# Performance work log

Measured on AMD Instinct MI355X. Metric: run time of the kernel, lower is better.

## Reference

```python
import jax, jax.numpy as jnp
import numpy as np

V, D, S, NL, B, L = 50257, 768, 16, 4, 2, 512
EPS = 1e-5

def _ln(x, g, b):
    m = x.mean(-1, keepdims=True)
    v = x.var(-1, keepdims=True)
    return (x - m) * jax.lax.rsqrt(v + EPS) * g + b

def setup_inputs() -> dict:
    key = jax.random.key(0)
    ks = jax.random.split(key, 10)
    def nrm(k, shape, s=0.02):
        return jax.random.normal(k, shape, jnp.float32) * s
    tokens = jax.random.randint(ks[0], (B, L), 0, V)
    return {
        "tokens": tokens,
        "emb": nrm(ks[1], (V, D)),
        "ln_g": jnp.ones((NL, D), jnp.float32),
        "ln_b": jnp.zeros((NL, D), jnp.float32),
        "in_w": nrm(ks[2], (NL, 2 * D, D)),        # torch Linear weight [out,in]
        "conv_w": nrm(ks[3], (NL, D, 3), 0.3),     # depthwise conv kernel [D,1,3] -> [D,3]
        "conv_b": jnp.zeros((NL, D), jnp.float32),
        "dt_w": nrm(ks[4], (NL, D, D)),
        "dt_b": jnp.zeros((NL, D), jnp.float32),
        "A_log": jax.random.normal(ks[5], (NL, D, S), jnp.float32),
        "D_param": jnp.ones((NL, D), jnp.float32),
        "out_w": nrm(ks[6], (NL, D, D)),
        "lnf_g": jnp.ones((D,), jnp.float32),
        "lnf_b": jnp.zeros((D,), jnp.float32),
        "head_w": nrm(ks[7], (V, D)),
    }

def _mamba_layer(x, p):
    g, b, inw, cw, cb, dtw, dtb, Al, Dd, ow = p
    xn = _ln(x, g, b)
    xr = jnp.einsum('bld,ed->ble', xn, inw)          # [B,L,2D]
    xi, res = xr[..., :D], xr[..., D:]
    # depthwise conv1d, kernel=3, padding=1 (cross-correlation, as torch)
    xp = jnp.pad(xi, ((0, 0), (1, 1), (0, 0)))
    xc = xp[:, :-2] * cw[:, 0] + xp[:, 1:-1] * cw[:, 1] + xp[:, 2:] * cw[:, 2] + cb
    xc = jax.nn.silu(xc)                              # [B,L,D]
    A = -jnp.exp(Al)                                  # [D,S]
    dt = jax.nn.sigmoid(jnp.einsum('bld,ed->ble', xc, dtw) + dtb)  # [B,L,D]
    decay = jnp.exp(A[None, None] * dt[..., None])    # [B,L,D,S]
    dec_t = jnp.moveaxis(decay, 1, 0)                 # [L,B,D,S]
    xc_t = jnp.moveaxis(xc, 1, 0)                     # [L,B,D]
    h0 = jnp.zeros((x.shape[0], D, S), x.dtype)
    def step(h, inp):
        dec, xt = inp
        h = h * dec + xt[..., None]
        return h, h.sum(-1)
    _, ys = jax.lax.scan(step, h0, (dec_t, xc_t))     # ys: [L,B,D]
    y = jnp.moveaxis(ys, 0, 1) * Dd                   # [B,L,D]
    y = y * jax.nn.silu(res)
    out = jnp.einsum('bld,ed->ble', y, ow)
    return x + out, None

def reference(tokens, emb, ln_g, ln_b, in_w, conv_w, conv_b, dt_w, dt_b,
              A_log, D_param, out_w, lnf_g, lnf_b, head_w):
    x = emb[tokens]                                   # [B,L,D]
    params = (ln_g, ln_b, in_w, conv_w, conv_b, dt_w, dt_b, A_log, D_param, out_w)
    x, _ = jax.lax.scan(_mamba_layer, x, params)      # scan over NL layers
    x = _ln(x, lnf_g, lnf_b)
    return jnp.einsum('bld,vd->blv', x, head_w)       # [B,L,V]
```

## Files before the change

### kernel.cpp

```cpp
#include <hip/hip_runtime.h>
#include <math.h>

#define V_  50257
#define D_  768
#define S_  16
#define NL_ 4
#define B_  2
#define L_  512
#define EPS_ 1e-5f

static constexpr int BLD  = B_ * L_ * D_;
static constexpr int ROWS = B_ * L_;
static constexpr int VPAD = 50304;

typedef __bf16 bf16x8 __attribute__((ext_vector_type(8)));
typedef __bf16 bf16x4 __attribute__((ext_vector_type(4)));
typedef float  f32x4  __attribute__((ext_vector_type(4)));

__global__ __launch_bounds__(256)
void emb_kernel(const int* __restrict__ tok, const float* __restrict__ emb,
                float* __restrict__ x) {
    int i = blockIdx.x * 256 + threadIdx.x;
    if (i >= BLD) return;
    int d  = i % D_;
    int bl = i / D_;
    x[i] = emb[(size_t)tok[bl] * D_ + d];
}

__global__ __launch_bounds__(256)
void ln_split_kernel(const float* __restrict__ x, const float* __restrict__ g,
                     const float* __restrict__ b, __bf16* __restrict__ hi,
                     __bf16* __restrict__ lo) {
    int row = blockIdx.x;
    const float* xr = x + (size_t)row * D_;
    int t = threadIdx.x;
    float v0 = xr[t], v1 = xr[t + 256], v2 = xr[t + 512];
    float s1 = v0 + v1 + v2;
    float s2 = v0 * v0 + v1 * v1 + v2 * v2;
    for (int off = 32; off > 0; off >>= 1) {
        s1 += __shfl_down(s1, off);
        s2 += __shfl_down(s2, off);
    }
    __shared__ float red[8];
    __shared__ float mv[2];
    int wave = t >> 6, lane = t & 63;
    if (lane == 0) { red[wave] = s1; red[4 + wave] = s2; }
    __syncthreads();
    if (t == 0) {
        float a = red[0] + red[1] + red[2] + red[3];
        float c = red[4] + red[5] + red[6] + red[7];
        float mean = a / (float)D_;
        float var  = c / (float)D_ - mean * mean;
        mv[0] = mean;
        mv[1] = 1.f / sqrtf(var + EPS_);
    }
    __syncthreads();
    float mean = mv[0], inv = mv[1];
    size_t o = (size_t)row * D_;
#pragma unroll
    for (int q = 0; q < 3; ++q) {
        int c = t + q * 256;
        float v = (q == 0 ? v0 : q == 1 ? v1 : v2);
        float n = (v - mean) * inv * g[c] + b[c];
        __bf16 h = (__bf16)n;
        hi[o + c] = h;
        lo[o + c] = (__bf16)(n - (float)h);
    }
}

__global__ __launch_bounds__(256)
void ln_kernel(const float* __restrict__ x, const float* __restrict__ g,
               const float* __restrict__ b, float* __restrict__ o) {
    int row = blockIdx.x;
    const float* xr = x + (size_t)row * D_;
    int t = threadIdx.x;
    float v0 = xr[t], v1 = xr[t + 256], v2 = xr[t + 512];
    float s1 = v0 + v1 + v2;
    float s2 = v0 * v0 + v1 * v1 + v2 * v2;
    for (int off = 32; off > 0; off >>= 1) {
        s1 += __shfl_down(s1, off);
        s2 += __shfl_down(s2, off);
    }
    __shared__ float red[8];
    __shared__ float mv[2];
    int wave = t >> 6, lane = t & 63;
    if (lane == 0) { red[wave] = s1; red[4 + wave] = s2; }
    __syncthreads();
    if (t == 0) {
        float a = red[0] + red[1] + red[2] + red[3];
        float c = red[4] + red[5] + red[6] + red[7];
        float mean = a / (float)D_;
        float var  = c / (float)D_ - mean * mean;
        mv[0] = mean;
        mv[1] = 1.f / sqrtf(var + EPS_);
    }
    __syncthreads();
    float mean = mv[0], inv = mv[1];
    float* orow = o + (size_t)row * D_;
    orow[t]       = (v0 - mean) * inv * g[t]       + b[t];
    orow[t + 256] = (v1 - mean) * inv * g[t + 256] + b[t + 256];
    orow[t + 512] = (v2 - mean) * inv * g[t + 512] + b[t + 512];
}

__global__ __launch_bounds__(256)
void conv_silu_split_kernel(const float* __restrict__ xr, const float* __restrict__ cw,
                            const float* __restrict__ cb, float* __restrict__ xc,
                            __bf16* __restrict__ hi, __bf16* __restrict__ lo) {
    int i = blockIdx.x * 256 + threadIdx.x;
    if (i >= BLD) return;
    int d  = i % D_;
    int bl = i / D_;
    int l  = bl % L_;
    const size_t stride = 2 * D_;
    float xm = (l > 0)      ? xr[(size_t)(bl - 1) * stride + d] : 0.f;
    float x0 =                xr[(size_t)bl * stride + d];
    float xp = (l < L_ - 1) ? xr[(size_t)(bl + 1) * stride + d] : 0.f;
    float v = xm * cw[d * 3 + 0] + x0 * cw[d * 3 + 1] + xp * cw[d * 3 + 2] + cb[d];
    float s = v / (1.f + __expf(-v));
    xc[i] = s;
    __bf16 h = (__bf16)s;
    hi[i] = h;
    lo[i] = (__bf16)(s - (float)h);
}

__global__ __launch_bounds__(256)
void conv_silu_kernel(const float* __restrict__ xr, const float* __restrict__ cw,
                      const float* __restrict__ cb, float* __restrict__ xc) {
    int i = blockIdx.x * 256 + threadIdx.x;
    if (i >= BLD) return;
    int d  = i % D_;
    int bl = i / D_;
    int l  = bl % L_;
    const size_t stride = 2 * D_;
    float xm = (l > 0)      ? xr[(size_t)(bl - 1) * stride + d] : 0.f;
    float x0 =                xr[(size_t)bl * stride + d];
    float xp = (l < L_ - 1) ? xr[(size_t)(bl + 1) * stride + d] : 0.f;
    float v = xm * cw[d * 3 + 0] + x0 * cw[d * 3 + 1] + xp * cw[d * 3 + 2] + cb[d];
    xc[i] = v / (1.f + __expf(-v));
}

__global__ __launch_bounds__(256)
void scan2_kernel(const float* __restrict__ dt, const float* __restrict__ xc,
                  const float* __restrict__ xr, const float* __restrict__ A_log,
                  const float* __restrict__ Dp, __bf16* __restrict__ yh,
                  __bf16* __restrict__ yl) {
    const int tid = threadIdx.x;
    const int s  = tid & 15;
    const int dd = (tid >> 4) & 1;
    const int c  = tid >> 5;
    const int dg = blockIdx.x % (D_ / 2);
    const int b  = blockIdx.x / (D_ / 2);
    const int d  = dg * 2 + dd;
    const float a = -__expf(A_log[d * S_ + s]);
    const int l0 = c * (L_ / 8);
    const float* dtp = dt + (size_t)b * L_ * D_ + d;
    const float* xcp = xc + (size_t)b * L_ * D_ + d;

    float P = 1.f, H = 0.f;
#pragma unroll 4
    for (int i = 0; i < L_ / 8; ++i) {
        float dtv = dtp[(size_t)(l0 + i) * D_];
        float xcv = xcp[(size_t)(l0 + i) * D_];
        float dec = __expf(a * dtv);
        P *= dec;
        H = H * dec + xcv;
    }
    __shared__ float Ps[8][2][16], Hs[8][2][16], HIn[8][2][16];
    Ps[c][dd][s] = P;
    Hs[c][dd][s] = H;
    __syncthreads();
    if (tid < 32) {
        int ss = tid & 15, d2 = tid >> 4;
        float carry = 0.f;
#pragma unroll
        for (int cc = 0; cc < 8; ++cc) {
            HIn[cc][d2][ss] = carry;
            carry = Hs[cc][d2][ss] + Ps[cc][d2][ss] * carry;
        }
    }
    __syncthreads();
    float h = HIn[c][dd][s];
    const float Dd = Dp[d];
    const float* rsp = xr + (size_t)b * L_ * 2 * D_ + D_ + d;
    size_t ybase = (size_t)b * L_ * D_ + d;
#pragma unroll 4
    for (int i = 0; i < L_ / 8; ++i) {
        int l = l0 + i;
        float dtv = dtp[(size_t)l * D_];
        float xcv = xcp[(size_t)l * D_];
        h = h * __expf(a * dtv) + xcv;
        float ys = h;
        ys += __shfl_xor(ys, 1, 16);
        ys += __shfl_xor(ys, 2, 16);
        ys += __shfl_xor(ys, 4, 16);
        ys += __shfl_xor(ys, 8, 16);
        if (s == 0) {
            float rv = rsp[(size_t)l * 2 * D_];
            float sil = rv / (1.f + __expf(-rv));
            float val = ys * Dd * sil;
            __bf16 hh = (__bf16)val;
            yh[ybase + (size_t)l * D_] = hh;
            yl[ybase + (size_t)l * D_] = (__bf16)(val - (float)hh);
        }
    }
}

__global__ __launch_bounds__(256)
void scan_kernel(const float* __restrict__ dt, const float* __restrict__ xc,
                 const float* __restrict__ xr, const float* __restrict__ A_log,
                 const float* __restrict__ Dp, float* __restrict__ y) {
    int t = blockIdx.x * 256 + threadIdx.x;
    int s = t & (S_ - 1);
    int d = (t >> 4) % D_;
    int b = t / (D_ * S_);
    float a  = -__expf(A_log[d * S_ + s]);
    float Dd = Dp[d];
    const float* dtp = dt + (size_t)b * L_ * D_ + d;
    const float* xcp = xc + (size_t)b * L_ * D_ + d;
    const float* rsp = xr + (size_t)b * L_ * 2 * D_ + D_ + d;
    float* yp = y + (size_t)b * L_ * D_ + d;
    float h = 0.f;
    for (int l = 0; l < L_; ++l) {
        float dtv = dtp[(size_t)l * D_];
        float xcv = xcp[(size_t)l * D_];
        h = h * __expf(a * dtv) + xcv;
        float ys = h;
        ys += __shfl_xor(ys, 1, 16);
        ys += __shfl_xor(ys, 2, 16);
        ys += __shfl_xor(ys, 4, 16);
        ys += __shfl_xor(ys, 8, 16);
        if (s == 0) {
            float rv = rsp[(size_t)l * 2 * D_];
            float sil = rv / (1.f + __expf(-rv));
            yp[(size_t)l * D_] = ys * Dd * sil;
        }
    }
}

__global__ __launch_bounds__(256)
void split4_kernel(const float* __restrict__ x, __bf16* __restrict__ hi,
                   __bf16* __restrict__ lo, int n4, int npad4) {
    int i = blockIdx.x * 256 + threadIdx.x;
    if (i >= npad4) return;
    float4 v = {0.f, 0.f, 0.f, 0.f};
    if (i < n4) v = ((const float4*)x)[i];
    bf16x4 h, l;
    h[0] = (__bf16)v.x; h[1] = (__bf16)v.y; h[2] = (__bf16)v.z; h[3] = (__bf16)v.w;
    l[0] = (__bf16)(v.x - (float)h[0]);
    l[1] = (__bf16)(v.y - (float)h[1]);
    l[2] = (__bf16)(v.z - (float)h[2]);
    l[3] = (__bf16)(v.w - (float)h[3]);
    *(bf16x4*)&hi[(size_t)i * 4] = h;
    *(bf16x4*)&lo[(size_t)i * 4] = l;
}

template <int BMt, int BNt, int EPI>
__global__ __launch_bounds__(256)
void gemm3(const __bf16* __restrict__ Ahi, const __bf16* __restrict__ Alo,
           const __bf16* __restrict__ Whi, const __bf16* __restrict__ Wlo,
           const float* __restrict__ bias, const float* __restrict__ resid,
           float* __restrict__ C, int N, int K, int gx) {
    constexpr int BK  = 32;
    constexpr int FR  = BMt / 32;
    constexpr int FC  = BNt / 32;
    constexpr int ASZ = BMt * BK;
    constexpr int WSZ = BNt * BK;
    __shared__ __bf16 Ah[2 * ASZ];
    __shared__ __bf16 Al[2 * ASZ];
    __shared__ __bf16 Wh[2 * WSZ];
    __shared__ __bf16 Wl[2 * WSZ];
    const int tid  = threadIdx.x;
    const int lane = tid & 63;
    const int wv   = tid >> 6;
    const int wr   = wv >> 1, wc = wv & 1;

    const int bid = blockIdx.x;
    const int nwg = gridDim.x;
    const int q = nwg >> 3, r = nwg & 7;
    const int xcd = bid & 7, lid = bid >> 3;
    const int swz = (xcd < r ? xcd * (q + 1) : r * (q + 1) + (xcd - r) * q) + lid;
    const int bm = (swz % gx) * BMt;
    const int bn = (swz / gx) * BNt;

    const int srow = tid >> 2;
    const int scol = (tid & 3) * 8;

    f32x4 acc[FR][FC] = {};

    const int arow = wr * (BMt / 2) + (lane & 15);
    const int brow = wc * (BNt / 2) + (lane & 15);
    const int kof  = (lane >> 4) * 8;

    auto STAGE = [&](int t) {
        const int k0  = t * BK;
        const int buf = t & 1;
#pragma unroll
        for (int i = 0; i < BMt / 64; ++i) {
            size_t go = (size_t)(bm + i * 64 + srow) * K + k0 + scol;
            __builtin_amdgcn_global_load_lds(
                (const __attribute__((address_space(1))) void*)(Ahi + go),
                (__attribute__((address_space(3))) void*)(Ah + buf * ASZ + i * 2048 + tid * 8),
                16, 0, 0);
            __builtin_amdgcn_global_load_lds(
                (const __attribute__((address_space(1))) void*)(Alo + go),
                (__attribute__((address_space(3))) void*)(Al + buf * ASZ + i * 2048 + tid * 8),
                16, 0, 0);
        }
#pragma unroll
        for (int i = 0; i < BNt / 64; ++i) {
            size_t go = (size_t)(bn + i * 64 + srow) * K + k0 + scol;
            __builtin_amdgcn_global_load_lds(
                (const __attribute__((address_space(1))) void*)(Whi + go),
                (__attribute__((address_space(3))) void*)(Wh + buf * WSZ + i * 2048 + tid * 8),
                16, 0, 0);
            __builtin_amdgcn_global_load_lds(
                (const __attribute__((address_space(1))) void*)(Wlo + go),
                (__attribute__((address_space(3))) void*)(Wl + buf * WSZ + i * 2048 + tid * 8),
                16, 0, 0);
        }
    };

    STAGE(0);
    const int nt = K / BK;
    for (int t = 0; t < nt; ++t) {
        __syncthreads();
        if (t + 1 < nt) STAGE(t + 1);
        const int buf = t & 1;
        const __bf16* Ahb = Ah + buf * ASZ;
        const __bf16* Alb = Al + buf * ASZ;
        const __bf16* Whb = Wh + buf * WSZ;
        const __bf16* Wlb = Wl + buf * WSZ;

        bf16x8 afh[FR], afl[FR], wfh[FC], wfl[FC];
#pragma unroll
        for (int f = 0; f < FR; ++f) {
            afh[f] = *(const bf16x8*)&Ahb[(arow + f * 16) * BK + kof];
            afl[f] = *(const bf16x8*)&Alb[(arow + f * 16) * BK + kof];
        }
#pragma unroll
        for (int f = 0; f < FC; ++f) {
            wfh[f] = *(const bf16x8*)&Whb[(brow + f * 16) * BK + kof];
            wfl[f] = *(const bf16x8*)&Wlb[(brow + f * 16) * BK + kof];
        }
#pragma unroll
        for (int i = 0; i < FR; ++i)
#pragma unroll
            for (int j = 0; j < FC; ++j) {
                acc[i][j] = __builtin_amdgcn_mfma_f32_16x16x32_bf16(
                    afh[i], wfh[j], acc[i][j], 0, 0, 0);
                acc[i][j] = __builtin_amdgcn_mfma_f32_16x16x32_bf16(
                    afl[i], wfh[j], acc[i][j], 0, 0, 0);
                acc[i][j] = __builtin_amdgcn_mfma_f32_16x16x32_bf16(
                    afh[i], wfl[j], acc[i][j], 0, 0, 0);
            }
    }

    const int rbase = bm + wr * (BMt / 2) + (lane >> 4) * 4;
    const int cbase = bn + wc * (BNt / 2) + (lane & 15);
#pragma unroll
    for (int i = 0; i < FR; ++i) {
#pragma unroll
        for (int j = 0; j < FC; ++j) {
#pragma unroll
            for (int r2 = 0; r2 < 4; ++r2) {
                int row = rbase + i * 16 + r2;
                int col = cbase + j * 16;
                if (col < N) {
                    float v = acc[i][j][r2];
                    if (EPI == 1) v = 1.f / (1.f + __expf(-(v + bias[col])));
                    if (EPI == 2) v = v + resid[(size_t)row * N + col];
                    C[(size_t)row * N + col] = v;
                }
            }
        }
    }
}

#define BM 128
#define BN 128
#define BKF 16

template <int EPI>
__global__ __launch_bounds__(256)
void gemm_wt(const float* __restrict__ A, const float* __restrict__ W,
             const float* __restrict__ bias, const float* __restrict__ resid,
             float* __restrict__ C, int M, int N, int K) {
    __shared__ float As[BKF][BM + 4];
    __shared__ float Wsh[BKF][BN + 4];
    const int tid = threadIdx.x;
    const int bm = blockIdx.y * BM;
    const int bn = blockIdx.x * BN;
    const int tx = tid & 15, ty = tid >> 4;
    const int lrow = tid >> 1;
    const int lk   = (tid & 1) * 8;
    float acc[8][8];
#pragma unroll
    for (int i = 0; i < 8; ++i)
#pragma unroll
        for (int j = 0; j < 8; ++j) acc[i][j] = 0.f;
    for (int k0 = 0; k0 < K; k0 += BKF) {
        const float* ap = A + (size_t)(bm + lrow) * K + k0 + lk;
        float4 av0 = *(const float4*)ap;
        float4 av1 = *(const float4*)(ap + 4);
        float4 wv0 = {0, 0, 0, 0}, wv1 = {0, 0, 0, 0};
        int wrow = bn + lrow;
        if (wrow < N) {
            const float* wp = W + (size_t)wrow * K + k0 + lk;
            wv0 = *(const float4*)wp;
            wv1 = *(const float4*)(wp + 4);
        }
        __syncthreads();
        As[lk + 0][lrow] = av0.x; As[lk + 1][lrow] = av0.y;
        As[lk + 2][lrow] = av0.z; As[lk + 3][lrow] = av0.w;
        As[lk + 4][lrow] = av1.x; As[lk + 5][lrow] = av1.y;
        As[lk + 6][lrow] = av1.z; As[lk + 7][lrow] = av1.w;
        Wsh[lk + 0][lrow] = wv0.x; Wsh[lk + 1][lrow] = wv0.y;
        Wsh[lk + 2][lrow] = wv0.z; Wsh[lk + 3][lrow] = wv0.w;
        Wsh[lk + 4][lrow] = wv1.x; Wsh[lk + 5][lrow] = wv1.y;
        Wsh[lk + 6][lrow] = wv1.z; Wsh[lk + 7][lrow] = wv1.w;
        __syncthreads();
#pragma unroll
        for (int k = 0; k < BKF; ++k) {
            float4 a0 = *(const float4*)&As[k][ty * 8];
            float4 a1 = *(const float4*)&As[k][ty * 8 + 4];
            float4 w0 = *(const float4*)&Wsh[k][tx * 8];
            float4 w1 = *(const float4*)&Wsh[k][tx * 8 + 4];
            float av[8] = {a0.x, a0.y, a0.z, a0.w, a1.x, a1.y, a1.z, a1.w};
            float wv[8] = {w0.x, w0.y, w0.z, w0.w, w1.x, w1.y, w1.z, w1.w};
#pragma unroll
            for (int i = 0; i < 8; ++i)
#pragma unroll
                for (int j = 0; j < 8; ++j)
                    acc[i][j] = fmaf(av[i], wv[j], acc[i][j]);
        }
    }
#pragma unroll
    for (int i = 0; i < 8; ++i) {
        int row = bm + ty * 8 + i;
#pragma unroll
        for (int j = 0; j < 8; ++j) {
            int col = bn + tx * 8 + j;
            if (col < N) {
                float v = acc[i][j];
                if (EPI == 1) v = 1.f / (1.f + expf(-(v + bias[col])));
                if (EPI == 2) v = v + resid[(size_t)row * N + col];
                C[(size_t)row * N + col] = v;
            }
        }
    }
}

extern "C" void kernel_launch(void* const* d_in, const int* in_sizes, int n_in,
                              void* d_out, int out_size, void* d_ws, size_t ws_size,
                              hipStream_t stream) {
    (void)in_sizes; (void)n_in; (void)out_size;
    const int*   tokens  = (const int*)  d_in[0];
    const float* emb     = (const float*)d_in[1];
    const float* ln_g    = (const float*)d_in[2];
    const float* ln_b    = (const float*)d_in[3];
    const float* in_w    = (const float*)d_in[4];
    const float* conv_w  = (const float*)d_in[5];
    const float* conv_b  = (const float*)d_in[6];
    const float* dt_w    = (const float*)d_in[7];
    const float* dt_b    = (const float*)d_in[8];
    const float* A_log   = (const float*)d_in[9];
    const float* D_param = (const float*)d_in[10];
    const float* out_w   = (const float*)d_in[11];
    const float* lnf_g   = (const float*)d_in[12];
    const float* lnf_b   = (const float*)d_in[13];
    const float* head_w  = (const float*)d_in[14];
    float* out = (float*)d_out;

    char* base = (char*)d_ws;
    char* p = base;
    auto alloc = [&](size_t bytes) -> char* {
        char* r = p;
        p += (bytes + 255) & ~(size_t)255;
        return r;
    };
    float* x  = (float*)alloc((size_t)BLD * 4);
    float* xn = (float*)alloc((size_t)BLD * 4);
    float* xr = (float*)alloc((size_t)2 * BLD * 4);
    float* xc = (float*)alloc((size_t)BLD * 4);
    float* dt = (float*)alloc((size_t)BLD * 4);
    float* y  = xn;
    size_t fb_need = (size_t)(p - base);

    __bf16* a_hi = (__bf16*)alloc((size_t)BLD * 2);
    __bf16* a_lo = (__bf16*)alloc((size_t)BLD * 2);
    const size_t INW = (size_t)NL_ * 2 * D_ * D_;
    const size_t SQW = (size_t)NL_ * D_ * D_;
    const size_t HW  = (size_t)VPAD * D_;
    __bf16* inw_hi  = (__bf16*)alloc(INW * 2);
    __bf16* inw_lo  = (__bf16*)alloc(INW * 2);
    __bf16* dtw_hi  = (__bf16*)alloc(SQW * 2);
    __bf16* dtw_lo  = (__bf16*)alloc(SQW * 2);
    __bf16* outw_hi = (__bf16*)alloc(SQW * 2);
    __bf16* outw_lo = (__bf16*)alloc(SQW * 2);
    __bf16* hw_hi   = (__bf16*)alloc(HW * 2);
    __bf16* hw_lo   = (__bf16*)alloc(HW * 2);
    size_t fast_need = (size_t)(p - base);

    const bool fast = ws_size >= fast_need && fb_need <= ws_size;

    emb_kernel<<<(BLD + 255) / 256, 256, 0, stream>>>(tokens, emb, x);

    if (fast) {
        int n4;
        n4 = (int)(INW / 4);
        split4_kernel<<<(n4 + 255) / 256, 256, 0, stream>>>(in_w, inw_hi, inw_lo, n4, n4);
        n4 = (int)(SQW / 4);
        split4_kernel<<<(n4 + 255) / 256, 256, 0, stream>>>(dt_w, dtw_hi, dtw_lo, n4, n4);
        split4_kernel<<<(n4 + 255) / 256, 256, 0, stream>>>(out_w, outw_hi, outw_lo, n4, n4);
        {
            int hn4 = (int)((size_t)V_ * D_ / 4), hp4 = (int)(HW / 4);
            split4_kernel<<<(hp4 + 255) / 256, 256, 0, stream>>>(head_w, hw_hi, hw_lo, hn4, hp4);
        }

        for (int l = 0; l < NL_; ++l) {
            const float* lg = ln_g + (size_t)l * D_;
            const float* lb = ln_b + (size_t)l * D_;
            const float* cw = conv_w + (size_t)l * D_ * 3;
            const float* cb = conv_b + (size_t)l * D_;
            const float* db = dt_b + (size_t)l * D_;
            const float* al = A_log + (size_t)l * D_ * S_;
            const float* dp = D_param + (size_t)l * D_;
            const __bf16* iwh = inw_hi + (size_t)l * 2 * D_ * D_;
            const __bf16* iwl = inw_lo + (size_t)l * 2 * D_ * D_;
            const __bf16* dwh = dtw_hi + (size_t)l * D_ * D_;
            const __bf16* dwl = dtw_lo + (size_t)l * D_ * D_;
            const __bf16* owh = outw_hi + (size_t)l * D_ * D_;
            const __bf16* owl = outw_lo + (size_t)l * D_ * D_;

            ln_split_kernel<<<ROWS, 256, 0, stream>>>(x, lg, lb, a_hi, a_lo);
            gemm3<64, 128, 0><<<(ROWS / 64) * (2 * D_ / 128), 256, 0, stream>>>(
                a_hi, a_lo, iwh, iwl, nullptr, nullptr, xr, 2 * D_, D_, ROWS / 64);
            conv_silu_split_kernel<<<(BLD + 255) / 256, 256, 0, stream>>>(
                xr, cw, cb, xc, a_hi, a_lo);
            gemm3<64, 64, 1><<<(ROWS / 64) * (D_ / 64), 256, 0, stream>>>(
                a_hi, a_lo, dwh, dwl, db, nullptr, dt, D_, D_, ROWS / 64);
            scan2_kernel<<<B_ * (D_ / 2), 256, 0, stream>>>(
                dt, xc, xr, al, dp, a_hi, a_lo);
            gemm3<64, 64, 2><<<(ROWS / 64) * (D_ / 64), 256, 0, stream>>>(
                a_hi, a_lo, owh, owl, nullptr, x, x, D_, D_, ROWS / 64);
        }

        ln_split_kernel<<<ROWS, 256, 0, stream>>>(x, lnf_g, lnf_b, a_hi, a_lo);
        gemm3<128, 128, 0><<<(ROWS / 128) * (VPAD / 128), 256, 0, stream>>>(
            a_hi, a_lo, hw_hi, hw_lo, nullptr, nullptr, out, V_, D_, ROWS / 128);
    } else {
        for (int l = 0; l < NL_; ++l) {
            const float* lg = ln_g + (size_t)l * D_;
            const float* lb = ln_b + (size_t)l * D_;
            const float* iw = in_w + (size_t)l * 2 * D_ * D_;
            const float* cw = conv_w + (size_t)l * D_ * 3;
            const float* cb = conv_b + (size_t)l * D_;
            const float* dw = dt_w + (size_t)l * D_ * D_;
            const float* db = dt_b + (size_t)l * D_;
            const float* al = A_log + (size_t)l * D_ * S_;
            const float* dp = D_param + (size_t)l * D_;
            const float* ow = out_w + (size_t)l * D_ * D_;
            ln_kernel<<<ROWS, 256, 0, stream>>>(x, lg, lb, xn);
            gemm_wt<0><<<dim3((2 * D_) / BN, ROWS / BM), 256, 0, stream>>>(
                xn, iw, nullptr, nullptr, xr, ROWS, 2 * D_, D_);
            conv_silu_kernel<<<(BLD + 255) / 256, 256, 0, stream>>>(xr, cw, cb, xc);
            gemm_wt<1><<<dim3(D_ / BN, ROWS / BM), 256, 0, stream>>>(
                xc, dw, db, nullptr, dt, ROWS, D_, D_);
            scan_kernel<<<(B_ * D_ * S_) / 256, 256, 0, stream>>>(
                dt, xc, xr, al, dp, y);
            gemm_wt<2><<<dim3(D_ / BN, ROWS / BM), 256, 0, stream>>>(
                y, ow, nullptr, x, x, ROWS, D_, D_);
        }
        ln_kernel<<<ROWS, 256, 0, stream>>>(x, lnf_g, lnf_b, xn);
        gemm_wt<0><<<dim3((V_ + BN - 1) / BN, ROWS / BM), 256, 0, stream>>>(
            xn, head_w, nullptr, nullptr, out, ROWS, V_, D_);
    }
}
```

Before: 1.273 ms.

## Fuse embedding with first LN, merge weight splits, widen scan and GEMM K-tile

Merges the four weight hi/lo split launches into one kernel and fuses the embedding gather with the first layer's layernorm split. The scan kernel now uses 16 chunks with 512 threads and keeps decay and input values in registers, so the second pass no longer reloads and recomputes them. The per-layer GEMMs use a 64-wide K tile, which halves the number of main-loop iterations. These changes cut launch count and memory traffic, at the cost of more registers in the scan and more LDS in the GEMMs.

Measured after the change: 1.171 ms. 1.09x faster.

```diff
diff --git a/kernel.cpp b/kernel.cpp
--- a/kernel.cpp
+++ b/kernel.cpp
@@ -25,6 +25,49 @@
     int d  = i % D_;
     int bl = i / D_;
     x[i] = emb[(size_t)tok[bl] * D_ + d];
+}
+
+__global__ __launch_bounds__(256)
+void emb_ln_split_kernel(const int* __restrict__ tok, const float* __restrict__ emb,
+                         const float* __restrict__ g, const float* __restrict__ b,
+                         float* __restrict__ x, __bf16* __restrict__ hi,
+                         __bf16* __restrict__ lo) {
+    int row = blockIdx.x;
+    const float* er = emb + (size_t)tok[row] * D_;
+    int t = threadIdx.x;
+    float v0 = er[t], v1 = er[t + 256], v2 = er[t + 512];
+    float s1 = v0 + v1 + v2;
+    float s2 = v0 * v0 + v1 * v1 + v2 * v2;
+    for (int off = 32; off > 0; off >>= 1) {
+        s1 += __shfl_down(s1, off);
+        s2 += __shfl_down(s2, off);
+    }
+    __shared__ float red[8];
+    __shared__ float mv[2];
+    int wave = t >> 6, lane = t & 63;
+    if (lane == 0) { red[wave] = s1; red[4 + wave] = s2; }
+    __syncthreads();
+    if (t == 0) {
+        float a = red[0] + red[1] + red[2] + red[3];
+        float c = red[4] + red[5] + red[6] + red[7];
+        float mean = a / (float)D_;
+        float var  = c / (float)D_ - mean * mean;
+        mv[0] = mean;
+        mv[1] = 1.f / sqrtf(var + EPS_);
+    }
+    __syncthreads();
+    float mean = mv[0], inv = mv[1];
+    size_t o = (size_t)row * D_;
+#pragma unroll
+    for (int q = 0; q < 3; ++q) {
+        int c = t + q * 256;
+        float v = (q == 0 ? v0 : q == 1 ? v1 : v2);
+        x[o + c] = v;
+        float n = (v - mean) * inv * g[c] + b[c];
+        __bf16 h = (__bf16)n;
+        hi[o + c] = h;
+        lo[o + c] = (__bf16)(n - (float)h);
+    }
 }
 
 __global__ __launch_bounds__(256)
@@ -139,11 +182,13 @@
     xc[i] = v / (1.f + __expf(-v));
 }
 
-__global__ __launch_bounds__(256)
-void scan2_kernel(const float* __restrict__ dt, const float* __restrict__ xc,
+__global__ __launch_bounds__(512)
+void scan3_kernel(const float* __restrict__ dt, const float* __restrict__ xc,
                   const float* __restrict__ xr, const float* __restrict__ A_log,
                   const float* __restrict__ Dp, __bf16* __restrict__ yh,
                   __bf16* __restrict__ yl) {
+    constexpr int NC = 16;
+    constexpr int CH = L_ / NC;
     const int tid = threadIdx.x;
     const int s  = tid & 15;
     const int dd = (tid >> 4) & 1;
@@ -152,20 +197,22 @@
     const int b  = blockIdx.x / (D_ / 2);
     const int d  = dg * 2 + dd;
     const float a = -__expf(A_log[d * S_ + s]);
-    const int l0 = c * (L_ / 8);
+    const int l0 = c * CH;
     const float* dtp = dt + (size_t)b * L_ * D_ + d;
     const float* xcp = xc + (size_t)b * L_ * D_ + d;
 
+    float dec[CH], xv[CH];
     float P = 1.f, H = 0.f;
-#pragma unroll 4
-    for (int i = 0; i < L_ / 8; ++i) {
+#pragma unroll
+    for (int i = 0; i < CH; ++i) {
         float dtv = dtp[(size_t)(l0 + i) * D_];
-        float xcv = xcp[(size_t)(l0 + i) * D_];
-        float dec = __expf(a * dtv);
-        P *= dec;
-        H = H * dec + xcv;
-    }
-    __shared__ float Ps[8][2][16], Hs[8][2][16], HIn[8][2][16];
+        float x0  = xcp[(size_t)(l0 + i) * D_];
+        float de  = __expf(a * dtv);
+        dec[i] = de; xv[i] = x0;
+        P *= de;
+        H = H * de + x0;
+    }
+    __shared__ float Ps[NC][2][16], Hs[NC][2][16], HIn[NC][2][16];
     Ps[c][dd][s] = P;
     Hs[c][dd][s] = H;
     __syncthreads();
@@ -173,7 +220,7 @@
         int ss = tid & 15, d2 = tid >> 4;
         float carry = 0.f;
 #pragma unroll
-        for (int cc = 0; cc < 8; ++cc) {
+        for (int cc = 0; cc < NC; ++cc) {
             HIn[cc][d2][ss] = carry;
             carry = Hs[cc][d2][ss] + Ps[cc][d2][ss] * carry;
         }
@@ -183,18 +230,16 @@
     const float Dd = Dp[d];
     const float* rsp = xr + (size_t)b * L_ * 2 * D_ + D_ + d;
     size_t ybase = (size_t)b * L_ * D_ + d;
-#pragma unroll 4
-    for (int i = 0; i < L_ / 8; ++i) {
-        int l = l0 + i;
-        float dtv = dtp[(size_t)l * D_];
-        float xcv = xcp[(size_t)l * D_];
-        h = h * __expf(a * dtv) + xcv;
+#pragma unroll
+    for (int i = 0; i < CH; ++i) {
+        h = h * dec[i] + xv[i];
         float ys = h;
         ys += __shfl_xor(ys, 1, 16);
         ys += __shfl_xor(ys, 2, 16);
         ys += __shfl_xor(ys, 4, 16);
         ys += __shfl_xor(ys, 8, 16);
         if (s == 0) {
+            int l = l0 + i;
             float rv = rsp[(size_t)l * 2 * D_];
             float sil = rv / (1.f + __expf(-rv));
             float val = ys * Dd * sil;
@@ -237,34 +282,57 @@
     }
 }
 
-__global__ __launch_bounds__(256)
-void split4_kernel(const float* __restrict__ x, __bf16* __restrict__ hi,
-                   __bf16* __restrict__ lo, int n4, int npad4) {
+static constexpr int N4_IN  = (int)((size_t)NL_ * 2 * D_ * D_ / 4);
+static constexpr int N4_SQ  = (int)((size_t)NL_ * D_ * D_ / 4);
+static constexpr int N4_HWP = (int)((size_t)VPAD * D_ / 4);
+static constexpr int N4_HW  = (int)((size_t)V_ * D_ / 4);
+static constexpr int T0 = N4_IN;
+static constexpr int T1 = T0 + N4_SQ;
+static constexpr int T2 = T1 + N4_SQ;
+static constexpr int T3 = T2 + N4_HWP;
+
+__global__ __launch_bounds__(256)
+void split_all_kernel(const float* __restrict__ inw, const float* __restrict__ dtw,
+                      const float* __restrict__ outw, const float* __restrict__ hw,
+                      __bf16* __restrict__ inh, __bf16* __restrict__ inl,
+                      __bf16* __restrict__ dth, __bf16* __restrict__ dtl,
+                      __bf16* __restrict__ oth, __bf16* __restrict__ otl,
+                      __bf16* __restrict__ hwh, __bf16* __restrict__ hwl) {
     int i = blockIdx.x * 256 + threadIdx.x;
-    if (i >= npad4) return;
+    if (i >= T3) return;
+    const float* src;
+    __bf16 *dh, *dl;
+    int j;
+    bool valid = true;
+    if (i < T0)      { j = i;      src = inw;  dh = inh; dl = inl; }
+    else if (i < T1) { j = i - T0; src = dtw;  dh = dth; dl = dtl; }
+    else if (i < T2) { j = i - T1; src = outw; dh = oth; dl = otl; }
+    else             { j = i - T2; src = hw;   dh = hwh; dl = hwl;
+                       valid = j < N4_HW; }
     float4 v = {0.f, 0.f, 0.f, 0.f};
-    if (i < n4) v = ((const float4*)x)[i];
+    if (valid) v = ((const float4*)src)[j];
     bf16x4 h, l;
     h[0] = (__bf16)v.x; h[1] = (__bf16)v.y; h[2] = (__bf16)v.z; h[3] = (__bf16)v.w;
     l[0] = (__bf16)(v.x - (float)h[0]);
     l[1] = (__bf16)(v.y - (float)h[1]);
     l[2] = (__bf16)(v.z - (float)h[2]);
     l[3] = (__bf16)(v.w - (float)h[3]);
-    *(bf16x4*)&hi[(size_t)i * 4] = h;
-    *(bf16x4*)&lo[(size_t)i * 4] = l;
-}
-
-template <int BMt, int BNt, int EPI>
+    *(bf16x4*)&dh[(size_t)j * 4] = h;
+    *(bf16x4*)&dl[(size_t)j * 4] = l;
+}
+
+template <int BMt, int BNt, int BK, int EPI>
 __global__ __launch_bounds__(256)
 void gemm3(const __bf16* __restrict__ Ahi, const __bf16* __restrict__ Alo,
            const __bf16* __restrict__ Whi, const __bf16* __restrict__ Wlo,
            const float* __restrict__ bias, const float* __restrict__ resid,
            float* __restrict__ C, int N, int K, int gx) {
-    constexpr int BK  = 32;
     constexpr int FR  = BMt / 32;
     constexpr int FC  = BNt / 32;
     constexpr int ASZ = BMt * BK;
     constexpr int WSZ = BNt * BK;
+    constexpr int NIA = ASZ / 2048;
+    constexpr int NIW = WSZ / 2048;
     __shared__ __bf16 Ah[2 * ASZ];
     __shared__ __bf16 Al[2 * ASZ];
     __shared__ __bf16 Wh[2 * WSZ];
@@ -282,9 +350,6 @@
     const int bm = (swz % gx) * BMt;
     const int bn = (swz / gx) * BNt;
 
-    const int srow = tid >> 2;
-    const int scol = (tid & 3) * 8;
-
     f32x4 acc[FR][FC] = {};
 
     const int arow = wr * (BMt / 2) + (lane & 15);
@@ -295,27 +360,31 @@
         const int k0  = t * BK;
         const int buf = t & 1;
 #pragma unroll
-        for (int i = 0; i < BMt / 64; ++i) {
-            size_t go = (size_t)(bm + i * 64 + srow) * K + k0 + scol;
+        for (int i = 0; i < NIA; ++i) {
+            int e = i * 2048 + tid * 8;
+            int row = e / BK, col = e % BK;
+            size_t go = (size_t)(bm + row) * K + k0 + col;
             __builtin_amdgcn_global_load_lds(
                 (const __attribute__((address_space(1))) void*)(Ahi + go),
-                (__attribute__((address_space(3))) void*)(Ah + buf * ASZ + i * 2048 + tid * 8),
+                (__attribute__((address_space(3))) void*)(Ah + buf * ASZ + e),
                 16, 0, 0);
             __builtin_amdgcn_global_load_lds(
                 (const __attribute__((address_space(1))) void*)(Alo + go),
-                (__attribute__((address_space(3))) void*)(Al + buf * ASZ + i * 2048 + tid * 8),
+                (__attribute__((address_space(3))) void*)(Al + buf * ASZ + e),
                 16, 0, 0);
         }
 #pragma unroll
-        for (int i = 0; i < BNt / 64; ++i) {
-            size_t go = (size_t)(bn + i * 64 + srow) * K + k0 + scol;
+        for (int i = 0; i < NIW; ++i) {
+            int e = i * 2048 + tid * 8;
+            int row = e / BK, col = e % BK;
+            size_t go = (size_t)(bn + row) * K + k0 + col;
             __builtin_amdgcn_global_load_lds(
                 (const __attribute__((address_space(1))) void*)(Whi + go),
-                (__attribute__((address_space(3))) void*)(Wh + buf * WSZ + i * 2048 + tid * 8),
+                (__attribute__((address_space(3))) void*)(Wh + buf * WSZ + e),
                 16, 0, 0);
             __builtin_amdgcn_global_load_lds(
                 (const __attribute__((address_space(1))) void*)(Wlo + go),
-                (__attribute__((address_space(3))) void*)(Wl + buf * WSZ + i * 2048 + tid * 8),
+                (__attribute__((address_space(3))) void*)(Wl + buf * WSZ + e),
                 16, 0, 0);
         }
     };
@@ -331,28 +400,31 @@
         const __bf16* Whb = Wh + buf * WSZ;
         const __bf16* Wlb = Wl + buf * WSZ;
 
-        bf16x8 afh[FR], afl[FR], wfh[FC], wfl[FC];
-#pragma unroll
-        for (int f = 0; f < FR; ++f) {
-            afh[f] = *(const bf16x8*)&Ahb[(arow + f * 16) * BK + kof];
-            afl[f] = *(const bf16x8*)&Alb[(arow + f * 16) * BK + kof];
-        }
-#pragma unroll
-        for (int f = 0; f < FC; ++f) {
-            wfh[f] = *(const bf16x8*)&Whb[(brow + f * 16) * BK + kof];
-            wfl[f] = *(const bf16x8*)&Wlb[(brow + f * 16) * BK + kof];
-        }
-#pragma unroll
-        for (int i = 0; i < FR; ++i)
-#pragma unroll
-            for (int j = 0; j < FC; ++j) {
-                acc[i][j] = __builtin_amdgcn_mfma_f32_16x16x32_bf16(
-                    afh[i], wfh[j], acc[i][j], 0, 0, 0);
-                acc[i][j] = __builtin_amdgcn_mfma_f32_16x16x32_bf16(
-                    afl[i], wfh[j], acc[i][j], 0, 0, 0);
-                acc[i][j] = __builtin_amdgcn_mfma_f32_16x16x32_bf16(
-                    afh[i], wfl[j], acc[i][j], 0, 0, 0);
+#pragma unroll
+        for (int kk = 0; kk < BK; kk += 32) {
+            bf16x8 afh[FR], afl[FR], wfh[FC], wfl[FC];
+#pragma unroll
+            for (int f = 0; f < FR; ++f) {
+                afh[f] = *(const bf16x8*)&Ahb[(arow + f * 16) * BK + kk + kof];
+                afl[f] = *(const bf16x8*)&Alb[(arow + f * 16) * BK + kk + kof];
             }
+#pragma unroll
+            for (int f = 0; f < FC; ++f) {
+                wfh[f] = *(const bf16x8*)&Whb[(brow + f * 16) * BK + kk + kof];
+                wfl[f] = *(const bf16x8*)&Wlb[(brow + f * 16) * BK + kk + kof];
+            }
+#pragma unroll
+            for (int i = 0; i < FR; ++i)
+#pragma unroll
+                for (int j = 0; j < FC; ++j) {
+                    acc[i][j] = __builtin_amdgcn_mfma_f32_16x16x32_bf16(
+                        afh[i], wfh[j], acc[i][j], 0, 0, 0);
+                    acc[i][j] = __builtin_amdgcn_mfma_f32_16x16x32_bf16(
+                        afl[i], wfh[j], acc[i][j], 0, 0, 0);
+                    acc[i][j] = __builtin_amdgcn_mfma_f32_16x16x32_bf16(
+                        afh[i], wfl[j], acc[i][j], 0, 0, 0);
+                }
+        }
     }
 
     const int rbase = bm + wr * (BMt / 2) + (lane >> 4) * 4;
@@ -503,19 +575,12 @@
 
     const bool fast = ws_size >= fast_need && fb_need <= ws_size;
 
-    emb_kernel<<<(BLD + 255) / 256, 256, 0, stream>>>(tokens, emb, x);
-
     if (fast) {
-        int n4;
-        n4 = (int)(INW / 4);
-        split4_kernel<<<(n4 + 255) / 256, 256, 0, stream>>>(in_w, inw_hi, inw_lo, n4, n4);
-        n4 = (int)(SQW / 4);
-        split4_kernel<<<(n4 + 255) / 256, 256, 0, stream>>>(dt_w, dtw_hi, dtw_lo, n4, n4);
-        split4_kernel<<<(n4 + 255) / 256, 256, 0, stream>>>(out_w, outw_hi, outw_lo, n4, n4);
-        {
-            int hn4 = (int)((size_t)V_ * D_ / 4), hp4 = (int)(HW / 4);
-            split4_kernel<<<(hp4 + 255) / 256, 256, 0, stream>>>(head_w, hw_hi, hw_lo, hn4, hp4);
-        }
+        split_all_kernel<<<(T3 + 255) / 256, 256, 0, stream>>>(
+            in_w, dt_w, out_w, head_w,
+            inw_hi, inw_lo, dtw_hi, dtw_lo, outw_hi, outw_lo, hw_hi, hw_lo);
+        emb_ln_split_kernel<<<ROWS, 256, 0, stream>>>(
+            tokens, emb, ln_g, ln_b, x, a_hi, a_lo);
 
         for (int l = 0; l < NL_; ++l) {
             const float* lg = ln_g + (size_t)l * D_;
@@ -532,23 +597,25 @@
             const __bf16* owh = outw_hi + (size_t)l * D_ * D_;
             const __bf16* owl = outw_lo + (size_t)l * D_ * D_;
 
-            ln_split_kernel<<<ROWS, 256, 0, stream>>>(x, lg, lb, a_hi, a_lo);
-            gemm3<64, 128, 0><<<(ROWS / 64) * (2 * D_ / 128), 256, 0, stream>>>(
+            if (l > 0)
+                ln_split_kernel<<<ROWS, 256, 0, stream>>>(x, lg, lb, a_hi, a_lo);
+            gemm3<64, 128, 64, 0><<<(ROWS / 64) * (2 * D_ / 128), 256, 0, stream>>>(
                 a_hi, a_lo, iwh, iwl, nullptr, nullptr, xr, 2 * D_, D_, ROWS / 64);
             conv_silu_split_kernel<<<(BLD + 255) / 256, 256, 0, stream>>>(
                 xr, cw, cb, xc, a_hi, a_lo);
-            gemm3<64, 64, 1><<<(ROWS / 64) * (D_ / 64), 256, 0, stream>>>(
+            gemm3<64, 64, 64, 1><<<(ROWS / 64) * (D_ / 64), 256, 0, stream>>>(
                 a_hi, a_lo, dwh, dwl, db, nullptr, dt, D_, D_, ROWS / 64);
-            scan2_kernel<<<B_ * (D_ / 2), 256, 0, stream>>>(
+            scan3_kernel<<<B_ * (D_ / 2), 512, 0, stream>>>(
                 dt, xc, xr, al, dp, a_hi, a_lo);
-            gemm3<64, 64, 2><<<(ROWS / 64) * (D_ / 64), 256, 0, stream>>>(
+            gemm3<64, 64, 64, 2><<<(ROWS / 64) * (D_ / 64), 256, 0, stream>>>(
                 a_hi, a_lo, owh, owl, nullptr, x, x, D_, D_, ROWS / 64);
         }
 
         ln_split_kernel<<<ROWS, 256, 0, stream>>>(x, lnf_g, lnf_b, a_hi, a_lo);
-        gemm3<128, 128, 0><<<(ROWS / 128) * (VPAD / 128), 256, 0, stream>>>(
+        gemm3<128, 128, 32, 0><<<(ROWS / 128) * (VPAD / 128), 256, 0, stream>>>(
             a_hi, a_lo, hw_hi, hw_lo, nullptr, nullptr, out, V_, D_, ROWS / 128);
     } else {
+        emb_kernel<<<(BLD + 255) / 256, 256, 0, stream>>>(tokens, emb, x);
         for (int l = 0; l < NL_; ++l) {
             const float* lg = ln_g + (size_t)l * D_;
             const float* lb = ln_b + (size_t)l * D_;
```
